# Kernel tuning notes

Measured on AMD Instinct MI355X. Metric: run time of the kernel, lower is better.

The kernel has to match this reference:

```python
import jax, jax.numpy as jnp
import numpy as np

NUM_HEADS = 16
EMB = 1024
HEAD_DIM = EMB // NUM_HEADS


def setup_inputs() -> dict:
    key = jax.random.key(0)
    ks = jax.random.split(key, 9)
    N, L = 2, 2048
    return {
        "keys": jax.random.normal(ks[0], (N, L, EMB), dtype=jnp.float32),
        "queries": jax.random.normal(ks[1], (N, L, EMB), dtype=jnp.float32),
        "values": jax.random.normal(ks[2], (N, L, EMB), dtype=jnp.float32),
        "mask": jax.random.randint(ks[3], (N, L), 0, 2, dtype=jnp.int32),
        "Wk": jax.random.normal(ks[4], (HEAD_DIM, HEAD_DIM), dtype=jnp.float32) * 0.05,
        "Wq": jax.random.normal(ks[5], (HEAD_DIM, HEAD_DIM), dtype=jnp.float32) * 0.05,
        "Wv": jax.random.normal(ks[6], (HEAD_DIM, HEAD_DIM), dtype=jnp.float32) * 0.05,
        "Wo": jax.random.normal(ks[7], (EMB, EMB), dtype=jnp.float32) * 0.02,
        "bo": jax.random.normal(ks[8], (EMB,), dtype=jnp.float32) * 0.02,
    }


def reference(keys, queries, values, mask, Wk, Wq, Wv, Wo, bo):
    N, Q, E = queries.shape
    H, D = NUM_HEADS, HEAD_DIM
    # reshape to heads: [N, L, H, D]
    k = keys.reshape(N, -1, H, D) @ Wk.T
    q = queries.reshape(N, -1, H, D) @ Wq.T
    # faithful to source bug: values are the v-projection of the projected queries
    v = q @ Wv.T
    # energy: [N, H, Q, K]
    energy = jnp.einsum("nqhd,nkhd->nhqk", q, k)
    m = mask[:, None, None, :]  # [N,1,1,K]
    energy = jnp.where(m == 0, jnp.float32(-1e20), energy)
    p = jax.nn.softmax(energy / jnp.sqrt(jnp.float32(E)), axis=3)
    attn = jnp.einsum("nhqk,nkhd->nqhd", p, v).reshape(N, Q, E)
    return attn @ Wo.T + bo
```

## Files before the change

kernel.cpp:

```cpp
#include <hip/hip_runtime.h>
#include <hip/hip_bf16.h>
#include <cmath>

constexpr int N_ = 2;
constexpr int L_ = 2048;
constexpr int H_ = 16;
constexpr int E_ = 1024;
constexpr int ROWS_ = N_ * L_ * H_;
constexpr float KSCALE = 0.04508422002778010648f;

typedef __attribute__((ext_vector_type(8))) short bf16x8;
typedef __attribute__((ext_vector_type(4))) float f32x4;
typedef unsigned short ushort_t;
#define MFMA16(a, b, c) __builtin_amdgcn_mfma_f32_16x16x32_bf16(a, b, c, 0, 0, 0)

__device__ __forceinline__ unsigned short f2bf(float x) {
    union { float f; unsigned u; } v; v.f = x;
    return (unsigned short)((v.u + 0x7fffu + ((v.u >> 16) & 1u)) >> 16);
}
__device__ __forceinline__ unsigned pack2(float a, float b) {
    __hip_bfloat162 t = __float22bfloat162_rn(make_float2(a, b));
    union { __hip_bfloat162 h; unsigned u; } v; v.h = t;
    return v.u;
}

__global__ __launch_bounds__(256) void proj_kernel(
    const float* __restrict__ keys, const float* __restrict__ queries,
    const float* __restrict__ Wk, const float* __restrict__ Wq, const float* __restrict__ Wv,
    ushort_t* __restrict__ qo, ushort_t* __restrict__ ko, ushort_t* __restrict__ vto)
{
    constexpr int P = 72;
    __shared__ __align__(16) ushort_t Xq[64 * P];
    __shared__ __align__(16) ushort_t Xk[64 * P];
    __shared__ __align__(16) ushort_t Wqs[64 * P];
    __shared__ __align__(16) ushort_t Wks[64 * P];
    __shared__ __align__(16) ushort_t Wvs[64 * P];
    const int tid = threadIdx.x;
    const int lt = blockIdx.x & 31;
    const int h  = (blockIdx.x >> 5) & 15;
    const int n  = blockIdx.x >> 9;
    const int r0 = tid >> 4, c4 = (tid & 15) * 4;

#pragma unroll
    for (int j = 0; j < 4; ++j) {
        const int r = r0 + 16 * j;
        const size_t xoff = (size_t)(n * L_ + lt * 64 + r) * E_ + h * 64 + c4;
        const float4 xq = *(const float4*)&queries[xoff];
        const float4 xk = *(const float4*)&keys[xoff];
        const float4 wq = *(const float4*)&Wq[r * 64 + c4];
        const float4 wk = *(const float4*)&Wk[r * 64 + c4];
        const float4 wv = *(const float4*)&Wv[r * 64 + c4];
        *(uint2*)&Xq[r * P + c4]  = make_uint2(pack2(xq.x, xq.y), pack2(xq.z, xq.w));
        *(uint2*)&Xk[r * P + c4]  = make_uint2(pack2(xk.x, xk.y), pack2(xk.z, xk.w));
        *(uint2*)&Wqs[r * P + c4] = make_uint2(pack2(wq.x, wq.y), pack2(wq.z, wq.w));
        *(uint2*)&Wks[r * P + c4] = make_uint2(pack2(wk.x, wk.y), pack2(wk.z, wk.w));
        *(uint2*)&Wvs[r * P + c4] = make_uint2(pack2(wv.x, wv.y), pack2(wv.z, wv.w));
    }
    __syncthreads();

    const int wave = tid >> 6, lane = tid & 63;
    const int quad = lane >> 4, l16 = lane & 15;
    const int arow = (wave * 16 + l16) * P;
    const f32x4 zero = (f32x4){0.f, 0.f, 0.f, 0.f};

    bf16x8 a0 = *(const bf16x8*)&Xq[arow + quad * 8];
    bf16x8 a1 = *(const bf16x8*)&Xq[arow + 32 + quad * 8];
    bf16x8 c0 = *(const bf16x8*)&Xk[arow + quad * 8];
    bf16x8 c1 = *(const bf16x8*)&Xk[arow + 32 + quad * 8];
    f32x4 qf[4], kf[4];
#pragma unroll
    for (int nt = 0; nt < 4; ++nt) {
        const int brow = (nt * 16 + l16) * P;
        f32x4 acc = MFMA16(a0, *(const bf16x8*)&Wqs[brow + quad * 8], zero);
        qf[nt] = MFMA16(a1, *(const bf16x8*)&Wqs[brow + 32 + quad * 8], acc);
        acc = MFMA16(c0, *(const bf16x8*)&Wks[brow + quad * 8], zero);
        kf[nt] = MFMA16(c1, *(const bf16x8*)&Wks[brow + 32 + quad * 8], acc);
    }
    __syncthreads();

    const int crow = wave * 16 + quad * 4;
#pragma unroll
    for (int nt = 0; nt < 4; ++nt)
#pragma unroll
        for (int reg = 0; reg < 4; ++reg) {
            Xq[(crow + reg) * P + nt * 16 + l16]  = f2bf(qf[nt][reg]);
            Wqs[(crow + reg) * P + nt * 16 + l16] = f2bf(kf[nt][reg] * KSCALE);
        }
    asm volatile("s_waitcnt lgkmcnt(0)" ::: "memory");

    bf16x8 va0 = *(const bf16x8*)&Xq[arow + quad * 8];
    bf16x8 va1 = *(const bf16x8*)&Xq[arow + 32 + quad * 8];
    f32x4 vf[4];
#pragma unroll
    for (int nt = 0; nt < 4; ++nt) {
        const int brow = (nt * 16 + l16) * P;
        f32x4 acc = MFMA16(va0, *(const bf16x8*)&Wvs[brow + quad * 8], zero);
        vf[nt] = MFMA16(va1, *(const bf16x8*)&Wvs[brow + 32 + quad * 8], acc);
    }
#pragma unroll
    for (int nt = 0; nt < 4; ++nt)
#pragma unroll
        for (int reg = 0; reg < 4; ++reg)
            Xk[(nt * 16 + l16) * P + crow + reg] = f2bf(vf[nt][reg]);
    __syncthreads();

#pragma unroll
    for (int j = 0; j < 4; ++j) {
        const int r = r0 + 16 * j;
        const size_t qkoff = (size_t)(n * L_ + lt * 64 + r) * E_ + h * 64 + c4;
        *(uint2*)&qo[qkoff] = *(const uint2*)&Xq[r * P + c4];
        *(uint2*)&ko[qkoff] = *(const uint2*)&Wqs[r * P + c4];
        const size_t vtoff = ((size_t)(n * H_ + h) * 64 + r) * L_ + lt * 64 + c4;
        *(uint2*)&vto[vtoff] = *(const uint2*)&Xk[r * P + c4];
    }
}

__global__ __launch_bounds__(256) void attn_kernel(
    const ushort_t* __restrict__ q, const ushort_t* __restrict__ k,
    const ushort_t* __restrict__ vt, const float* __restrict__ maskf,
    ushort_t* __restrict__ attn)
{
    constexpr int P = 72;
    __shared__ __align__(16) ushort_t Ks[2][64 * P];
    __shared__ __align__(16) ushort_t VTs[2][64 * P];
    __shared__ __align__(16) ushort_t Ps[128 * P];
    __shared__ float Ls[128];

    const int g = blockIdx.x;
    const int xcd = g & 7, j0 = g >> 3;
    const int nh = xcd * 4 + (j0 & 3);
    const int qt = j0 >> 2;
    const int n = nh >> 4, h = nh & 15;

    const int tid = threadIdx.x;
    const int wave = tid >> 6, lane = tid & 63;
    const int l16 = lane & 15, quad = lane >> 4;
    const int r0 = tid >> 4, c4 = (tid & 15) * 4;

    const ushort_t* kh = k  + (size_t)n * L_ * E_ + h * 64;
    const ushort_t* vh = vt + (size_t)(n * H_ + h) * 64 * L_;
    const float*    mh = maskf + n * L_;
    const size_t qrow0 = (size_t)n * L_ + qt * 128 + wave * 32;

    bf16x8 qb[2][2];
#pragma unroll
    for (int s = 0; s < 2; ++s)
#pragma unroll
        for (int c = 0; c < 2; ++c)
            qb[s][c] = *(const bf16x8*)&q[(qrow0 + s * 16 + l16) * E_ + h * 64 + c * 32 + quad * 8];

    uint2 kr[4], vr[4];
#pragma unroll
    for (int j = 0; j < 4; ++j) {
        const int r = r0 + 16 * j;
        kr[j] = *(const uint2*)&kh[(size_t)r * E_ + c4];
        vr[j] = *(const uint2*)&vh[(size_t)r * L_ + c4];
    }
    f32x4 mf[4];
#pragma unroll
    for (int mk = 0; mk < 4; ++mk) mf[mk] = *(const f32x4*)&mh[mk * 16 + quad * 4];

#pragma unroll
    for (int j = 0; j < 4; ++j) {
        const int r = r0 + 16 * j;
        *(uint2*)&Ks[0][r * P + c4]  = kr[j];
        *(uint2*)&VTs[0][r * P + c4] = vr[j];
    }
    __syncthreads();

    float lacc[2] = {0.f, 0.f};
    f32x4 O[2][4];
#pragma unroll
    for (int s = 0; s < 2; ++s)
#pragma unroll
        for (int dt = 0; dt < 4; ++dt) O[s][dt] = (f32x4){0.f, 0.f, 0.f, 0.f};

    for (int t = 0; t < 32; ++t) {
        const int cur = t & 1, nxt = cur ^ 1;
        const int tn = (t < 31) ? t + 1 : 31;

#pragma unroll
        for (int j = 0; j < 4; ++j) {
            const int r = r0 + 16 * j;
            kr[j] = *(const uint2*)&kh[(size_t)(tn * 64 + r) * E_ + c4];
            vr[j] = *(const uint2*)&vh[(size_t)r * L_ + tn * 64 + c4];
        }
        f32x4 mfn[4];
#pragma unroll
        for (int mk = 0; mk < 4; ++mk)
            mfn[mk] = *(const f32x4*)&mh[tn * 64 + mk * 16 + quad * 4];

        bf16x8 kA[4][2];
#pragma unroll
        for (int mk = 0; mk < 4; ++mk)
#pragma unroll
            for (int c = 0; c < 2; ++c)
                kA[mk][c] = *(const bf16x8*)&Ks[cur][(mk * 16 + l16) * P + c * 32 + quad * 8];

        f32x4 sA[2][4];
#pragma unroll
        for (int s = 0; s < 2; ++s)
#pragma unroll
            for (int mk = 0; mk < 4; ++mk) {
                f32x4 acc = mf[mk];
                acc = MFMA16(kA[mk][0], qb[s][0], acc);
                sA[s][mk] = MFMA16(kA[mk][1], qb[s][1], acc);
            }

#pragma unroll
        for (int s = 0; s < 2; ++s)
#pragma unroll
            for (int mk = 0; mk < 4; ++mk) {
                const float p0 = __builtin_amdgcn_exp2f(sA[s][mk][0]);
                const float p1 = __builtin_amdgcn_exp2f(sA[s][mk][1]);
                const float p2 = __builtin_amdgcn_exp2f(sA[s][mk][2]);
                const float p3 = __builtin_amdgcn_exp2f(sA[s][mk][3]);
                lacc[s] += (p0 + p1) + (p2 + p3);
                *(uint2*)&Ps[(wave * 32 + s * 16 + l16) * P + mk * 16 + quad * 4] =
                    make_uint2(pack2(p0, p1), pack2(p2, p3));
            }
        asm volatile("s_waitcnt lgkmcnt(0)" ::: "memory");

        bf16x8 vB[4][2];
#pragma unroll
        for (int dt = 0; dt < 4; ++dt)
#pragma unroll
            for (int c = 0; c < 2; ++c)
                vB[dt][c] = *(const bf16x8*)&VTs[cur][(dt * 16 + l16) * P + c * 32 + quad * 8];
        bf16x8 pa[2][2];
#pragma unroll
        for (int s = 0; s < 2; ++s)
#pragma unroll
            for (int c = 0; c < 2; ++c)
                pa[s][c] = *(const bf16x8*)&Ps[(wave * 32 + s * 16 + l16) * P + c * 32 + quad * 8];
#pragma unroll
        for (int s = 0; s < 2; ++s)
#pragma unroll
            for (int dt = 0; dt < 4; ++dt) {
                O[s][dt] = MFMA16(pa[s][0], vB[dt][0], O[s][dt]);
                O[s][dt] = MFMA16(pa[s][1], vB[dt][1], O[s][dt]);
            }

#pragma unroll
        for (int j = 0; j < 4; ++j) {
            const int r = r0 + 16 * j;
            *(uint2*)&Ks[nxt][r * P + c4]  = kr[j];
            *(uint2*)&VTs[nxt][r * P + c4] = vr[j];
        }
#pragma unroll
        for (int mk = 0; mk < 4; ++mk) mf[mk] = mfn[mk];
        __syncthreads();
    }

#pragma unroll
    for (int s = 0; s < 2; ++s) {
        float v = lacc[s];
        v += __shfl_xor(v, 16);
        v += __shfl_xor(v, 32);
        if (quad == 0) Ls[wave * 32 + s * 16 + l16] = 1.f / v;
    }
    asm volatile("s_waitcnt lgkmcnt(0)" ::: "memory");
    f32x4 linv[2];
#pragma unroll
    for (int s = 0; s < 2; ++s) linv[s] = *(const f32x4*)&Ls[wave * 32 + s * 16 + quad * 4];

#pragma unroll
    for (int s = 0; s < 2; ++s)
#pragma unroll
        for (int dt = 0; dt < 4; ++dt)
#pragma unroll
            for (int reg = 0; reg < 4; ++reg) {
                const size_t row = qrow0 + s * 16 + quad * 4 + reg;
                attn[row * E_ + h * 64 + dt * 16 + l16] = f2bf(O[s][dt][reg] * linv[s][reg]);
            }
}

__global__ __launch_bounds__(256) void conv_misc_kernel(
    const float* __restrict__ Wo, const int* __restrict__ mask,
    ushort_t* __restrict__ Wob, float* __restrict__ maskf)
{
    if (blockIdx.x < 1024) {
        const int i = (blockIdx.x * 256 + threadIdx.x) * 4;
        const float4 w = *(const float4*)&Wo[i];
        *(uint2*)&Wob[i] = make_uint2(pack2(w.x, w.y), pack2(w.z, w.w));
    } else {
        const int j = (blockIdx.x - 1024) * 256 + threadIdx.x;
        if (j < N_ * L_) maskf[j] = mask[j] ? 0.f : -1e9f;
    }
}

__global__ __launch_bounds__(256) void outproj_kernel(
    const ushort_t* __restrict__ attn, const ushort_t* __restrict__ Wob,
    const float* __restrict__ bo, float* __restrict__ out)
{
    constexpr int P = 72;
    __shared__ __align__(16) ushort_t As[128 * P];
    __shared__ __align__(16) ushort_t Bs[64 * P];
    const int tid = threadIdx.x;
    const int bc = (blockIdx.x & 15) * 64;
    const int br = (blockIdx.x >> 4) * 128;
    const int r0 = tid >> 4, c4 = (tid & 15) * 4;
    const int wave = tid >> 6, lane = tid & 63;
    const int quad = lane >> 4, l16 = lane & 15;

    uint2 ar[8], brg[4];
#pragma unroll
    for (int j = 0; j < 8; ++j)
        ar[j] = *(const uint2*)&attn[(size_t)(br + r0 + 16 * j) * E_ + c4];
#pragma unroll
    for (int j = 0; j < 4; ++j)
        brg[j] = *(const uint2*)&Wob[(size_t)(bc + r0 + 16 * j) * E_ + c4];

    f32x4 acc[2][4];
#pragma unroll
    for (int s = 0; s < 2; ++s)
#pragma unroll
        for (int nt = 0; nt < 4; ++nt) acc[s][nt] = (f32x4){0.f, 0.f, 0.f, 0.f};

    for (int kt = 0; kt < 16; ++kt) {
#pragma unroll
        for (int j = 0; j < 8; ++j) *(uint2*)&As[(r0 + 16 * j) * P + c4] = ar[j];
#pragma unroll
        for (int j = 0; j < 4; ++j) *(uint2*)&Bs[(r0 + 16 * j) * P + c4] = brg[j];
        __syncthreads();
        const int knext = ((kt < 15) ? (kt + 1) : kt) * 64;
#pragma unroll
        for (int j = 0; j < 8; ++j)
            ar[j] = *(const uint2*)&attn[(size_t)(br + r0 + 16 * j) * E_ + knext + c4];
#pragma unroll
        for (int j = 0; j < 4; ++j)
            brg[j] = *(const uint2*)&Wob[(size_t)(bc + r0 + 16 * j) * E_ + knext + c4];

        bf16x8 aw[2][2], bw[4][2];
#pragma unroll
        for (int s = 0; s < 2; ++s)
#pragma unroll
            for (int c = 0; c < 2; ++c)
                aw[s][c] = *(const bf16x8*)&As[(wave * 32 + s * 16 + l16) * P + c * 32 + quad * 8];
#pragma unroll
        for (int nt = 0; nt < 4; ++nt)
#pragma unroll
            for (int c = 0; c < 2; ++c)
                bw[nt][c] = *(const bf16x8*)&Bs[(nt * 16 + l16) * P + c * 32 + quad * 8];
#pragma unroll
        for (int s = 0; s < 2; ++s)
#pragma unroll
            for (int nt = 0; nt < 4; ++nt) {
                acc[s][nt] = MFMA16(aw[s][0], bw[nt][0], acc[s][nt]);
                acc[s][nt] = MFMA16(aw[s][1], bw[nt][1], acc[s][nt]);
            }
        __syncthreads();
    }
#pragma unroll
    for (int s = 0; s < 2; ++s)
#pragma unroll
        for (int nt = 0; nt < 4; ++nt) {
            const float bias = bo[bc + nt * 16 + l16];
#pragma unroll
            for (int reg = 0; reg < 4; ++reg)
                out[(size_t)(br + wave * 32 + s * 16 + quad * 4 + reg) * E_ + bc + nt * 16 + l16] =
                    acc[s][nt][reg] + bias;
        }
}

extern "C" void kernel_launch(void* const* d_in, const int* in_sizes, int n_in,
                              void* d_out, int out_size, void* d_ws, size_t ws_size,
                              hipStream_t stream)
{
    const float* keys    = (const float*)d_in[0];
    const float* queries = (const float*)d_in[1];
    const int*   mask    = (const int*)d_in[3];
    const float* Wk      = (const float*)d_in[4];
    const float* Wq      = (const float*)d_in[5];
    const float* Wv      = (const float*)d_in[6];
    const float* Wo      = (const float*)d_in[7];
    const float* bo      = (const float*)d_in[8];
    float* out = (float*)d_out;

    ushort_t* qbf  = (ushort_t*)d_ws;
    ushort_t* kbf  = qbf + (size_t)ROWS_ * 64;
    ushort_t* vtbf = kbf + (size_t)ROWS_ * 64;
    ushort_t* abf  = vtbf + (size_t)ROWS_ * 64;
    ushort_t* wob  = abf + (size_t)ROWS_ * 64;
    float*    mskf = (float*)(wob + (size_t)E_ * E_);

    conv_misc_kernel<<<1024 + (N_ * L_ + 255) / 256, 256, 0, stream>>>(Wo, mask, wob, mskf);
    proj_kernel<<<N_ * H_ * (L_ / 64), 256, 0, stream>>>(keys, queries, Wk, Wq, Wv,
                                                         qbf, kbf, vtbf);
    attn_kernel<<<N_ * H_ * (L_ / 128), 256, 0, stream>>>(qbf, kbf, vtbf, mskf, abf);
    outproj_kernel<<<(N_ * L_ / 128) * (E_ / 64), 256, 0, stream>>>(abf, wob, bo, out);
}
```

Measured before the change: 194.2 us.

## Redistribute softmax probabilities in registers via permlane swaps instead of LDS

The P tile is no longer written to shared memory and read back as an MFMA A-operand. Instead the packed bf16 probabilities are rearranged across lanes with v_permlane32_swap and v_permlane16_swap. This removes the Ps LDS buffer, a store/load round-trip and an lgkmcnt wait per iteration. K/V tile loads are also widened from 8-byte to 16-byte vectors. The risk is that the register lane permutation must exactly match the MFMA operand layout to stay correct.

```diff
diff --git a/kernel.cpp b/kernel.cpp
--- a/kernel.cpp
+++ b/kernel.cpp
@@ -22,6 +22,12 @@
     __hip_bfloat162 t = __float22bfloat162_rn(make_float2(a, b));
     union { __hip_bfloat162 h; unsigned u; } v; v.h = t;
     return v.u;
+}
+__device__ __forceinline__ void plswap32(unsigned &a, unsigned &b) {
+    asm("v_permlane32_swap_b32 %0, %1" : "+v"(a), "+v"(b));
+}
+__device__ __forceinline__ void plswap16(unsigned &a, unsigned &b) {
+    asm("v_permlane16_swap_b32 %0, %1" : "+v"(a), "+v"(b));
 }
 
 __global__ __launch_bounds__(256) void proj_kernel(
@@ -123,7 +129,6 @@
     constexpr int P = 72;
     __shared__ __align__(16) ushort_t Ks[2][64 * P];
     __shared__ __align__(16) ushort_t VTs[2][64 * P];
-    __shared__ __align__(16) ushort_t Ps[128 * P];
     __shared__ float Ls[128];
 
     const int g = blockIdx.x;
@@ -135,7 +140,7 @@
     const int tid = threadIdx.x;
     const int wave = tid >> 6, lane = tid & 63;
     const int l16 = lane & 15, quad = lane >> 4;
-    const int r0 = tid >> 4, c4 = (tid & 15) * 4;
+    const int r8 = tid >> 3, c8 = (tid & 7) * 8;
 
     const ushort_t* kh = k  + (size_t)n * L_ * E_ + h * 64;
     const ushort_t* vh = vt + (size_t)(n * H_ + h) * 64 * L_;
@@ -149,22 +154,22 @@
         for (int c = 0; c < 2; ++c)
             qb[s][c] = *(const bf16x8*)&q[(qrow0 + s * 16 + l16) * E_ + h * 64 + c * 32 + quad * 8];
 
-    uint2 kr[4], vr[4];
-#pragma unroll
-    for (int j = 0; j < 4; ++j) {
-        const int r = r0 + 16 * j;
-        kr[j] = *(const uint2*)&kh[(size_t)r * E_ + c4];
-        vr[j] = *(const uint2*)&vh[(size_t)r * L_ + c4];
+    uint4 kr[2], vr[2];
+#pragma unroll
+    for (int j = 0; j < 2; ++j) {
+        const int r = r8 + 32 * j;
+        kr[j] = *(const uint4*)&kh[(size_t)r * E_ + c8];
+        vr[j] = *(const uint4*)&vh[(size_t)r * L_ + c8];
     }
     f32x4 mf[4];
 #pragma unroll
     for (int mk = 0; mk < 4; ++mk) mf[mk] = *(const f32x4*)&mh[mk * 16 + quad * 4];
 
 #pragma unroll
-    for (int j = 0; j < 4; ++j) {
-        const int r = r0 + 16 * j;
-        *(uint2*)&Ks[0][r * P + c4]  = kr[j];
-        *(uint2*)&VTs[0][r * P + c4] = vr[j];
+    for (int j = 0; j < 2; ++j) {
+        const int r = r8 + 32 * j;
+        *(uint4*)&Ks[0][r * P + c8]  = kr[j];
+        *(uint4*)&VTs[0][r * P + c8] = vr[j];
     }
     __syncthreads();
 
@@ -180,10 +185,10 @@
         const int tn = (t < 31) ? t + 1 : 31;
 
 #pragma unroll
-        for (int j = 0; j < 4; ++j) {
-            const int r = r0 + 16 * j;
-            kr[j] = *(const uint2*)&kh[(size_t)(tn * 64 + r) * E_ + c4];
-            vr[j] = *(const uint2*)&vh[(size_t)r * L_ + tn * 64 + c4];
+        for (int j = 0; j < 2; ++j) {
+            const int r = r8 + 32 * j;
+            kr[j] = *(const uint4*)&kh[(size_t)(tn * 64 + r) * E_ + c8];
+            vr[j] = *(const uint4*)&vh[(size_t)r * L_ + tn * 64 + c8];
         }
         f32x4 mfn[4];
 #pragma unroll
@@ -207,8 +212,17 @@
                 sA[s][mk] = MFMA16(kA[mk][1], qb[s][1], acc);
             }
 
-#pragma unroll
-        for (int s = 0; s < 2; ++s)
+        bf16x8 vB[4][2];
+#pragma unroll
+        for (int dt = 0; dt < 4; ++dt)
+#pragma unroll
+            for (int c = 0; c < 2; ++c)
+                vB[dt][c] = *(const bf16x8*)&VTs[cur][(dt * 16 + l16) * P + c * 32 + quad * 8];
+
+        bf16x8 pa[2][2];
+#pragma unroll
+        for (int s = 0; s < 2; ++s) {
+            unsigned u[4][2];
 #pragma unroll
             for (int mk = 0; mk < 4; ++mk) {
                 const float p0 = __builtin_amdgcn_exp2f(sA[s][mk][0]);
@@ -216,23 +230,23 @@
                 const float p2 = __builtin_amdgcn_exp2f(sA[s][mk][2]);
                 const float p3 = __builtin_amdgcn_exp2f(sA[s][mk][3]);
                 lacc[s] += (p0 + p1) + (p2 + p3);
-                *(uint2*)&Ps[(wave * 32 + s * 16 + l16) * P + mk * 16 + quad * 4] =
-                    make_uint2(pack2(p0, p1), pack2(p2, p3));
-            }
-        asm volatile("s_waitcnt lgkmcnt(0)" ::: "memory");
-
-        bf16x8 vB[4][2];
-#pragma unroll
-        for (int dt = 0; dt < 4; ++dt)
-#pragma unroll
-            for (int c = 0; c < 2; ++c)
-                vB[dt][c] = *(const bf16x8*)&VTs[cur][(dt * 16 + l16) * P + c * 32 + quad * 8];
-        bf16x8 pa[2][2];
-#pragma unroll
-        for (int s = 0; s < 2; ++s)
-#pragma unroll
-            for (int c = 0; c < 2; ++c)
-                pa[s][c] = *(const bf16x8*)&Ps[(wave * 32 + s * 16 + l16) * P + c * 32 + quad * 8];
+                u[mk][0] = pack2(p0, p1);
+                u[mk][1] = pack2(p2, p3);
+            }
+#pragma unroll
+            for (int c = 0; c < 2; ++c) {
+                union { unsigned w[4]; bf16x8 v; } pw;
+#pragma unroll
+                for (int hh = 0; hh < 2; ++hh) {
+                    unsigned a = u[2 * c][hh], b = u[2 * c + 1][hh];
+                    plswap32(a, b);
+                    plswap16(a, b);
+                    pw.w[hh] = a; pw.w[2 + hh] = b;
+                }
+                pa[s][c] = pw.v;
+            }
+        }
+
 #pragma unroll
         for (int s = 0; s < 2; ++s)
 #pragma unroll
@@ -242,10 +256,10 @@
             }
 
 #pragma unroll
-        for (int j = 0; j < 4; ++j) {
-            const int r = r0 + 16 * j;
-            *(uint2*)&Ks[nxt][r * P + c4]  = kr[j];
-            *(uint2*)&VTs[nxt][r * P + c4] = vr[j];
+        for (int j = 0; j < 2; ++j) {
+            const int r = r8 + 32 * j;
+            *(uint4*)&Ks[nxt][r * P + c8]  = kr[j];
+            *(uint4*)&VTs[nxt][r * P + c8] = vr[j];
         }
 #pragma unroll
         for (int mk = 0; mk < 4; ++mk) mf[mk] = mfn[mk];
```

Measured after the change: 201.4 us. 3.7% more time.

## Use 8 waves per attention block with 16 query rows per wave

Applied to the files above, without the earlier changes.

The attention kernel now launches 512 threads, so each of eight waves owns 16 query rows instead of four waves owning 32 rows each. Per-wave register use for scores, outputs and Q fragments drops by half. K/V tile loads widen from uint2 to uint4, with one load per thread per tile. The aim is more resident waves to hide latency. The cost is that each K/V LDS fragment is reused by fewer MFMAs per wave, and barriers now synchronize more waves.

```diff
diff --git a/kernel.cpp b/kernel.cpp
--- a/kernel.cpp
+++ b/kernel.cpp
@@ -115,7 +115,7 @@
     }
 }
 
-__global__ __launch_bounds__(256) void attn_kernel(
+__global__ __launch_bounds__(512, 4) void attn_kernel(
     const ushort_t* __restrict__ q, const ushort_t* __restrict__ k,
     const ushort_t* __restrict__ vt, const float* __restrict__ maskf,
     ushort_t* __restrict__ attn)
@@ -135,56 +135,39 @@
     const int tid = threadIdx.x;
     const int wave = tid >> 6, lane = tid & 63;
     const int l16 = lane & 15, quad = lane >> 4;
-    const int r0 = tid >> 4, c4 = (tid & 15) * 4;
+    const int rS = tid >> 3, cS = (tid & 7) * 8;
 
     const ushort_t* kh = k  + (size_t)n * L_ * E_ + h * 64;
     const ushort_t* vh = vt + (size_t)(n * H_ + h) * 64 * L_;
     const float*    mh = maskf + n * L_;
-    const size_t qrow0 = (size_t)n * L_ + qt * 128 + wave * 32;
-
-    bf16x8 qb[2][2];
-#pragma unroll
-    for (int s = 0; s < 2; ++s)
-#pragma unroll
-        for (int c = 0; c < 2; ++c)
-            qb[s][c] = *(const bf16x8*)&q[(qrow0 + s * 16 + l16) * E_ + h * 64 + c * 32 + quad * 8];
-
-    uint2 kr[4], vr[4];
-#pragma unroll
-    for (int j = 0; j < 4; ++j) {
-        const int r = r0 + 16 * j;
-        kr[j] = *(const uint2*)&kh[(size_t)r * E_ + c4];
-        vr[j] = *(const uint2*)&vh[(size_t)r * L_ + c4];
-    }
+    const size_t qrow0 = (size_t)n * L_ + qt * 128 + wave * 16;
+
+    bf16x8 qb[2];
+#pragma unroll
+    for (int c = 0; c < 2; ++c)
+        qb[c] = *(const bf16x8*)&q[(qrow0 + l16) * E_ + h * 64 + c * 32 + quad * 8];
+
+    uint4 kr = *(const uint4*)&kh[(size_t)rS * E_ + cS];
+    uint4 vr = *(const uint4*)&vh[(size_t)rS * L_ + cS];
     f32x4 mf[4];
 #pragma unroll
     for (int mk = 0; mk < 4; ++mk) mf[mk] = *(const f32x4*)&mh[mk * 16 + quad * 4];
 
-#pragma unroll
-    for (int j = 0; j < 4; ++j) {
-        const int r = r0 + 16 * j;
-        *(uint2*)&Ks[0][r * P + c4]  = kr[j];
-        *(uint2*)&VTs[0][r * P + c4] = vr[j];
-    }
+    *(uint4*)&Ks[0][rS * P + cS]  = kr;
+    *(uint4*)&VTs[0][rS * P + cS] = vr;
     __syncthreads();
 
-    float lacc[2] = {0.f, 0.f};
-    f32x4 O[2][4];
-#pragma unroll
-    for (int s = 0; s < 2; ++s)
-#pragma unroll
-        for (int dt = 0; dt < 4; ++dt) O[s][dt] = (f32x4){0.f, 0.f, 0.f, 0.f};
+    float lacc = 0.f;
+    f32x4 O[4];
+#pragma unroll
+    for (int dt = 0; dt < 4; ++dt) O[dt] = (f32x4){0.f, 0.f, 0.f, 0.f};
 
     for (int t = 0; t < 32; ++t) {
         const int cur = t & 1, nxt = cur ^ 1;
         const int tn = (t < 31) ? t + 1 : 31;
 
-#pragma unroll
-        for (int j = 0; j < 4; ++j) {
-            const int r = r0 + 16 * j;
-            kr[j] = *(const uint2*)&kh[(size_t)(tn * 64 + r) * E_ + c4];
-            vr[j] = *(const uint2*)&vh[(size_t)r * L_ + tn * 64 + c4];
-        }
+        kr = *(const uint4*)&kh[(size_t)(tn * 64 + rS) * E_ + cS];
+        vr = *(const uint4*)&vh[(size_t)rS * L_ + tn * 64 + cS];
         f32x4 mfn[4];
 #pragma unroll
         for (int mk = 0; mk < 4; ++mk)
@@ -197,28 +180,24 @@
             for (int c = 0; c < 2; ++c)
                 kA[mk][c] = *(const bf16x8*)&Ks[cur][(mk * 16 + l16) * P + c * 32 + quad * 8];
 
-        f32x4 sA[2][4];
-#pragma unroll
-        for (int s = 0; s < 2; ++s)
-#pragma unroll
-            for (int mk = 0; mk < 4; ++mk) {
-                f32x4 acc = mf[mk];
-                acc = MFMA16(kA[mk][0], qb[s][0], acc);
-                sA[s][mk] = MFMA16(kA[mk][1], qb[s][1], acc);
-            }
-
-#pragma unroll
-        for (int s = 0; s < 2; ++s)
-#pragma unroll
-            for (int mk = 0; mk < 4; ++mk) {
-                const float p0 = __builtin_amdgcn_exp2f(sA[s][mk][0]);
-                const float p1 = __builtin_amdgcn_exp2f(sA[s][mk][1]);
-                const float p2 = __builtin_amdgcn_exp2f(sA[s][mk][2]);
-                const float p3 = __builtin_amdgcn_exp2f(sA[s][mk][3]);
-                lacc[s] += (p0 + p1) + (p2 + p3);
-                *(uint2*)&Ps[(wave * 32 + s * 16 + l16) * P + mk * 16 + quad * 4] =
-                    make_uint2(pack2(p0, p1), pack2(p2, p3));
-            }
+        f32x4 sA[4];
+#pragma unroll
+        for (int mk = 0; mk < 4; ++mk) {
+            f32x4 acc = mf[mk];
+            acc = MFMA16(kA[mk][0], qb[0], acc);
+            sA[mk] = MFMA16(kA[mk][1], qb[1], acc);
+        }
+
+#pragma unroll
+        for (int mk = 0; mk < 4; ++mk) {
+            const float p0 = __builtin_amdgcn_exp2f(sA[mk][0]);
+            const float p1 = __builtin_amdgcn_exp2f(sA[mk][1]);
+            const float p2 = __builtin_amdgcn_exp2f(sA[mk][2]);
+            const float p3 = __builtin_amdgcn_exp2f(sA[mk][3]);
+            lacc += (p0 + p1) + (p2 + p3);
+            *(uint2*)&Ps[(wave * 16 + l16) * P + mk * 16 + quad * 4] =
+                make_uint2(pack2(p0, p1), pack2(p2, p3));
+        }
         asm volatile("s_waitcnt lgkmcnt(0)" ::: "memory");
 
         bf16x8 vB[4][2];
@@ -227,52 +206,39 @@
 #pragma unroll
             for (int c = 0; c < 2; ++c)
                 vB[dt][c] = *(const bf16x8*)&VTs[cur][(dt * 16 + l16) * P + c * 32 + quad * 8];
-        bf16x8 pa[2][2];
-#pragma unroll
-        for (int s = 0; s < 2; ++s)
-#pragma unroll
-            for (int c = 0; c < 2; ++c)
-                pa[s][c] = *(const bf16x8*)&Ps[(wave * 32 + s * 16 + l16) * P + c * 32 + quad * 8];
-#pragma unroll
-        for (int s = 0; s < 2; ++s)
-#pragma unroll
-            for (int dt = 0; dt < 4; ++dt) {
-                O[s][dt] = MFMA16(pa[s][0], vB[dt][0], O[s][dt]);
-                O[s][dt] = MFMA16(pa[s][1], vB[dt][1], O[s][dt]);
-            }
-
-#pragma unroll
-        for (int j = 0; j < 4; ++j) {
-            const int r = r0 + 16 * j;
-            *(uint2*)&Ks[nxt][r * P + c4]  = kr[j];
-            *(uint2*)&VTs[nxt][r * P + c4] = vr[j];
-        }
+        bf16x8 pa[2];
+#pragma unroll
+        for (int c = 0; c < 2; ++c)
+            pa[c] = *(const bf16x8*)&Ps[(wave * 16 + l16) * P + c * 32 + quad * 8];
+#pragma unroll
+        for (int dt = 0; dt < 4; ++dt) {
+            O[dt] = MFMA16(pa[0], vB[dt][0], O[dt]);
+            O[dt] = MFMA16(pa[1], vB[dt][1], O[dt]);
+        }
+
+        *(uint4*)&Ks[nxt][rS * P + cS]  = kr;
+        *(uint4*)&VTs[nxt][rS * P + cS] = vr;
 #pragma unroll
         for (int mk = 0; mk < 4; ++mk) mf[mk] = mfn[mk];
         __syncthreads();
     }
 
-#pragma unroll
-    for (int s = 0; s < 2; ++s) {
-        float v = lacc[s];
+    {
+        float v = lacc;
         v += __shfl_xor(v, 16);
         v += __shfl_xor(v, 32);
-        if (quad == 0) Ls[wave * 32 + s * 16 + l16] = 1.f / v;
+        if (quad == 0) Ls[wave * 16 + l16] = 1.f / v;
     }
     asm volatile("s_waitcnt lgkmcnt(0)" ::: "memory");
-    f32x4 linv[2];
-#pragma unroll
-    for (int s = 0; s < 2; ++s) linv[s] = *(const f32x4*)&Ls[wave * 32 + s * 16 + quad * 4];
-
-#pragma unroll
-    for (int s = 0; s < 2; ++s)
-#pragma unroll
-        for (int dt = 0; dt < 4; ++dt)
-#pragma unroll
-            for (int reg = 0; reg < 4; ++reg) {
-                const size_t row = qrow0 + s * 16 + quad * 4 + reg;
-                attn[row * E_ + h * 64 + dt * 16 + l16] = f2bf(O[s][dt][reg] * linv[s][reg]);
-            }
+    f32x4 linv = *(const f32x4*)&Ls[wave * 16 + quad * 4];
+
+#pragma unroll
+    for (int dt = 0; dt < 4; ++dt)
+#pragma unroll
+        for (int reg = 0; reg < 4; ++reg) {
+            const size_t row = qrow0 + quad * 4 + reg;
+            attn[row * E_ + h * 64 + dt * 16 + l16] = f2bf(O[dt][reg] * linv[reg]);
+        }
 }
 
 __global__ __launch_bounds__(256) void conv_misc_kernel(
@@ -387,6 +353,6 @@
     conv_misc_kernel<<<1024 + (N_ * L_ + 255) / 256, 256, 0, stream>>>(Wo, mask, wob, mskf);
     proj_kernel<<<N_ * H_ * (L_ / 64), 256, 0, stream>>>(keys, queries, Wk, Wq, Wv,
                                                          qbf, kbf, vtbf);
-    attn_kernel<<<N_ * H_ * (L_ / 128), 256, 0, stream>>>(qbf, kbf, vtbf, mskf, abf);
+    attn_kernel<<<N_ * H_ * (L_ / 128), 512, 0, stream>>>(qbf, kbf, vtbf, mskf, abf);
     outproj_kernel<<<(N_ * L_ / 128) * (E_ / 64), 256, 0, stream>>>(abf, wob, bo, out);
 }
```

Result: faster. 183.8 us (-5.4%).
